# Kernel optimization log

Hardware: AMD Instinct MI355X
Metric: run time of the kernel (lower is better)

## Reference

```python
import jax, jax.numpy as jnp
import numpy as np

B, S, R, L, Z = 2048, 277, 80, 12, 56


def setup_inputs() -> dict:
    key = jax.random.key(0)
    k0, k1, k2, k3, k4, k5 = jax.random.split(key, 6)
    true_idx = jax.random.randint(k0, (B, S), 0, R)
    x = jax.nn.one_hot(true_idx, R, dtype=jnp.float32)            # one-hot true rules
    recon_x = jax.nn.softmax(jax.random.normal(k1, (B, S, R)), axis=-1)  # post-softmax probs
    mu = jax.random.normal(k2, (B, Z), dtype=jnp.float32)
    log_var = jax.random.normal(k3, (B, Z), dtype=jnp.float32)
    ind_to_lhs_ind = jax.random.randint(k4, (R,), 0, L)
    masks = (jax.random.uniform(k5, (L, R)) > 0.5).astype(jnp.float32)
    # a valid grammar always allows the true rule under its own LHS mask
    masks = masks.at[ind_to_lhs_ind, jnp.arange(R)].set(1.0)
    return {"x": x, "recon_x": recon_x, "mu": mu, "log_var": log_var,
            "masks": masks, "ind_to_lhs_ind": ind_to_lhs_ind}


def reference(x, recon_x, mu, log_var, masks, ind_to_lhs_ind):
    batch_size, seq_len, n_rules = x.shape
    z_size = mu.shape[1]
    # apply_masks: fused gather + mask + renormalize (replaces B*S python loop)
    true_rule = jnp.argmax(x, axis=-1)                 # [B,S]
    mask = masks[ind_to_lhs_ind[true_rule]]            # [B,S,R]
    x_resc = recon_x * mask
    out = x_resc / jnp.sum(x_resc, axis=-1, keepdims=True)
    # BCELoss(size_average=False): torch clamps log terms at -100
    log_p = jnp.clip(jnp.log(out), -100.0, None)
    log_1mp = jnp.clip(jnp.log1p(-out), -100.0, None)
    bce = -jnp.sum(x * log_p + (1.0 - x) * log_1mp) / (seq_len * batch_size)
    # sample_z == False branch: moment-matching error
    avg_mu = jnp.sum(mu, axis=0) / batch_size          # [Z]
    var = jnp.matmul(mu.T, mu) / batch_size            # [Z,Z]
    var_err = var - jnp.eye(z_size, dtype=mu.dtype)
    mom_err = jnp.sum(avg_mu * avg_mu) / z_size + jnp.sum(jnp.abs(var_err)) / (z_size * z_size)
    return bce + mom_err
```

## Files before the change

### kernel.cpp

```cpp
#include <hip/hip_runtime.h>
#include <math.h>

#define Bn 2048
#define Sn 277
#define Rn 80
#define Ln 12
#define Zn 56
#define NROWS (Bn * Sn)
#define NBLK_BCE 2216
#define ITERS 4
#define NMOM 32
#define MROWS (Bn / NMOM)
#define NBLK_TOT (NBLK_BCE + NMOM)
#define NWAVE_BCE (NBLK_BCE * 4)

#define WS_CM  0
#define WS_BCE 1280
#define WS_VAR 36736
#define WS_AVG 49280

typedef float f4 __attribute__((ext_vector_type(4)));

__device__ __forceinline__ float qsum4(float v) {
    int t = __builtin_amdgcn_update_dpp(0, __float_as_int(v), 0xB1, 0xF, 0xF, true);
    v += __int_as_float(t);
    t = __builtin_amdgcn_update_dpp(0, __float_as_int(v), 0x4E, 0xF, 0xF, true);
    v += __int_as_float(t);
    return v;
}

__global__ __launch_bounds__(256) void setup_kernel(
    const float* __restrict__ masks, const int* __restrict__ lhs, char* __restrict__ ws)
{
    unsigned* cmask_sw = (unsigned*)(ws + WS_CM);
    for (int idx = threadIdx.x; idx < Rn * 4; idx += 256) {
        const int r = idx >> 2, c = idx & 3;
        const int l = lhs[r];
        unsigned bits = 0u;
        for (int k = 0; k < 5; ++k)
            for (int comp = 0; comp < 4; ++comp) {
                const int j = 16 * k + 4 * c + comp;
                if (masks[l * Rn + j] > 0.5f) bits |= (1u << (4 * k + comp));
            }
        cmask_sw[idx] = bits;
    }
}

__global__ __launch_bounds__(256, 4) void main_kernel(
    const float* __restrict__ x, const float* __restrict__ recon,
    const float* __restrict__ mu, char* __restrict__ ws)
{
    const int tid = threadIdx.x;

    if (blockIdx.x < NMOM) {
        __shared__ float sm[MROWS * Zn];
        float* var_g = (float*)(ws + WS_VAR);
        float* avg_g = (float*)(ws + WS_AVG);
        const int m = blockIdx.x;
        const float* src = mu + (size_t)m * MROWS * Zn;
        for (int i = tid; i < MROWS * Zn; i += 256) sm[i] = src[i];
        __syncthreads();

        #pragma unroll 1
        for (int k = 0; k < 13; ++k) {
            const int p = tid + 256 * k;
            if (p < Zn * Zn) {
                const int i = p / Zn, j = p - i * Zn;
                float a = 0.0f;
                #pragma unroll 8
                for (int r = 0; r < MROWS; ++r) a = fmaf(sm[r * Zn + i], sm[r * Zn + j], a);
                atomicAdd(&var_g[p], a);
            }
        }
        if (tid < Zn) {
            float s = 0.0f;
            #pragma unroll 8
            for (int r = 0; r < MROWS; ++r) s += sm[r * Zn + tid];
            atomicAdd(&avg_g[tid], s);
        }
        return;
    }

    const int bid = blockIdx.x - NMOM;
    const unsigned* cmask_sw = (const unsigned*)(ws + WS_CM);
    float* bce_partial = (float*)(ws + WS_BCE);

    const int q = tid >> 2;
    const int c = tid & 3;
    const f4* xp = (const f4*)x;
    const f4* rp = (const f4*)recon;
    int off = (bid * 256 + q) * 20 + c;

    auto dotc = [](const f4 v, float base_) {
        return fmaf(v.x, base_, fmaf(v.y, base_ + 1.f, fmaf(v.z, base_ + 2.f, v.w * (base_ + 3.f))));
    };

    float ss = 0.0f;
    #pragma unroll 1
    for (int it = 0; it < ITERS; ++it, off += 64 * 20) {
        f4 X[5], Rv[5];
        #pragma unroll
        for (int k = 0; k < 5; ++k) X[k]  = __builtin_nontemporal_load(&xp[off + 4 * k]);
        #pragma unroll
        for (int k = 0; k < 5; ++k) Rv[k] = __builtin_nontemporal_load(&rp[off + 4 * k]);
        __builtin_amdgcn_sched_barrier(0);

        float dl = dotc(X[0], 0.f) + dotc(X[1], 16.f) + dotc(X[2], 32.f)
                 + dotc(X[3], 48.f) + dotc(X[4], 64.f);
        float xs = 0.f;
        #pragma unroll
        for (int k = 0; k < 5; ++k)
            xs += ((X[k].x + X[k].y) + (X[k].z + X[k].w));
        dl = fmaf((float)(4 * c), xs, dl);
        const int amax = (int)(qsum4(dl) + 0.5f);

        const unsigned bits = cmask_sw[(amax << 2) | c];

        #pragma unroll
        for (int k = 0; k < 5; ++k) {
            Rv[k].x = ((bits >> (4 * k + 0)) & 1u) ? Rv[k].x : 0.f;
            Rv[k].y = ((bits >> (4 * k + 1)) & 1u) ? Rv[k].y : 0.f;
            Rv[k].z = ((bits >> (4 * k + 2)) & 1u) ? Rv[k].z : 0.f;
            Rv[k].w = ((bits >> (4 * k + 3)) & 1u) ? Rv[k].w : 0.f;
        }
        float dd = 0.f;
        #pragma unroll
        for (int k = 0; k < 5; ++k)
            dd += ((Rv[k].x + Rv[k].y) + (Rv[k].z + Rv[k].w));
        const float invd = __builtin_amdgcn_rcpf(qsum4(dd));

        const int ka = amax >> 4;
        const int ca = (amax >> 2) & 3;
        const int comp = amax & 3;
        const bool owner = (c == ca);

        float p = 1.0f;
        float ta = 1.0f;
        #pragma unroll
        for (int k = 0; k < 5; ++k) {
            const float t0 = fminf(Rv[k].x * invd, 1.f);
            const float t1 = fminf(Rv[k].y * invd, 1.f);
            const float t2 = fminf(Rv[k].z * invd, 1.f);
            const float t3 = fminf(Rv[k].w * invd, 1.f);
            p *= ((1.f - t0) * (1.f - t1)) * ((1.f - t2) * (1.f - t3));
            if (owner && k == ka)
                ta = (comp == 0) ? t0 : (comp == 1) ? t1 : (comp == 2) ? t2 : t3;
        }
        if (p > 0.0f) {
            ss += __builtin_amdgcn_logf(p) * 0.69314718055994531f;
        } else {
            #pragma unroll
            for (int k = 0; k < 5; ++k) {
                ss += fmaxf(__logf(1.f - fminf(Rv[k].x * invd, 1.f)), -100.f)
                    + fmaxf(__logf(1.f - fminf(Rv[k].y * invd, 1.f)), -100.f)
                    + fmaxf(__logf(1.f - fminf(Rv[k].z * invd, 1.f)), -100.f)
                    + fmaxf(__logf(1.f - fminf(Rv[k].w * invd, 1.f)), -100.f);
            }
        }
        if (owner)
            ss += fmaxf(__logf(ta), -100.f) - fmaxf(__logf(1.f - ta), -100.f);
    }

    ss = qsum4(ss);
    ss += __shfl_xor(ss, 4);
    ss += __shfl_xor(ss, 8);
    ss += __shfl_xor(ss, 16);
    ss += __shfl_xor(ss, 32);
    if ((tid & 63) == 0)
        bce_partial[bid * 4 + (tid >> 6)] = ss;
}

__global__ __launch_bounds__(256) void finalize_kernel(
    const char* __restrict__ ws, float* __restrict__ out)
{
    const float* bce_partial = (const float*)(ws + WS_BCE);
    const float* var_g = (const float*)(ws + WS_VAR);
    const float* avg_g = (const float*)(ws + WS_AVG);
    __shared__ double sb[4];
    __shared__ float sv[4], sa[4];
    const int tid = threadIdx.x;

    double bsum = 0.0;
    for (int i = tid; i < NWAVE_BCE; i += 256) bsum += (double)bce_partial[i];

    float vsum = 0.0f;
    for (int p = tid; p < Zn * Zn; p += 256) {
        const int i = p / Zn, j = p - i * Zn;
        const float e = var_g[p] * (1.0f / (float)Bn) - ((i == j) ? 1.0f : 0.0f);
        vsum += fabsf(e);
    }
    float asum = 0.0f;
    for (int z = tid; z < Zn; z += 256) { const float a = avg_g[z]; asum += a * a; }

    #pragma unroll
    for (int o = 32; o; o >>= 1) {
        bsum += __shfl_xor(bsum, o);
        vsum += __shfl_xor(vsum, o);
        asum += __shfl_xor(asum, o);
    }
    if ((tid & 63) == 0) { const int w = tid >> 6; sb[w] = bsum; sv[w] = vsum; sa[w] = asum; }
    __syncthreads();
    if (tid == 0) {
        const double tb = (sb[0] + sb[1]) + (sb[2] + sb[3]);
        const double tv = (double)((sv[0] + sv[1]) + (sv[2] + sv[3]));
        const double ta = (double)((sa[0] + sa[1]) + (sa[2] + sa[3]));
        const double bce = -tb / ((double)Sn * (double)Bn);
        const double mom = ta / ((double)Bn * (double)Bn * (double)Zn)
                         + tv / ((double)Zn * (double)Zn);
        out[0] = (float)(bce + mom);
    }
}

extern "C" void kernel_launch(void* const* d_in, const int* in_sizes, int n_in,
                              void* d_out, int out_size, void* d_ws, size_t ws_size,
                              hipStream_t stream)
{
    const float* x     = (const float*)d_in[0];
    const float* recon = (const float*)d_in[1];
    const float* mu    = (const float*)d_in[2];
    const float* masks = (const float*)d_in[4];
    const int*   lhs   = (const int*)d_in[5];
    float* out = (float*)d_out;
    char* ws = (char*)d_ws;

    hipMemsetAsync(ws + WS_VAR, 0, 12544 + 224, stream);
    setup_kernel<<<1, 256, 0, stream>>>(masks, lhs, ws);
    main_kernel<<<NBLK_TOT, 256, 0, stream>>>(x, recon, mu, ws);
    finalize_kernel<<<1, 256, 0, stream>>>(ws, out);
}
```

Baseline: 361.9 us.

## Stage BCE tiles through LDS with fully coalesced loads, one tile per block

Each BCE block now handles 64 rows in a single pass instead of looping four times. It loads x and recon with fully contiguous per-thread float4 accesses, stages them in padded LDS (stride 21) to avoid bank conflicts, then reads them back in the row-per-quad layout. Partial sums are reduced per block through LDS, so there is one partial per block instead of one per wave. The aim is better global coalescing and more blocks in flight. The cost is 43KB of LDS per block, a lower occupancy hint (3), and an extra LDS round trip and barriers.

```diff
diff --git a/kernel.cpp b/kernel.cpp
--- a/kernel.cpp
+++ b/kernel.cpp
@@ -7,12 +7,11 @@
 #define Ln 12
 #define Zn 56
 #define NROWS (Bn * Sn)
-#define NBLK_BCE 2216
-#define ITERS 4
+#define ROWS_PER_BLK 64
+#define NBLK_BCE (NROWS / ROWS_PER_BLK)
 #define NMOM 32
 #define MROWS (Bn / NMOM)
 #define NBLK_TOT (NBLK_BCE + NMOM)
-#define NWAVE_BCE (NBLK_BCE * 4)
 
 #define WS_CM  0
 #define WS_BCE 1280
@@ -46,16 +45,17 @@
     }
 }
 
-__global__ __launch_bounds__(256, 4) void main_kernel(
+__global__ __launch_bounds__(256, 3) void main_kernel(
     const float* __restrict__ x, const float* __restrict__ recon,
     const float* __restrict__ mu, char* __restrict__ ws)
 {
+    __shared__ f4 ldsb[2688];
     const int tid = threadIdx.x;
 
     if (blockIdx.x < NMOM) {
-        __shared__ float sm[MROWS * Zn];
         float* var_g = (float*)(ws + WS_VAR);
         float* avg_g = (float*)(ws + WS_AVG);
+        float* sm = (float*)ldsb;
         const int m = blockIdx.x;
         const float* src = mu + (size_t)m * MROWS * Zn;
         for (int i = tid; i < MROWS * Zn; i += 256) sm[i] = src[i];
@@ -85,26 +85,40 @@
     const unsigned* cmask_sw = (const unsigned*)(ws + WS_CM);
     float* bce_partial = (float*)(ws + WS_BCE);
 
-    const int q = tid >> 2;
-    const int c = tid & 3;
-    const f4* xp = (const f4*)x;
-    const f4* rp = (const f4*)recon;
-    int off = (bid * 256 + q) * 20 + c;
+    const size_t base = (size_t)bid * (ROWS_PER_BLK * (Rn / 4));
+    const f4* xg = (const f4*)x + base;
+    const f4* rg = (const f4*)recon + base;
+
+    f4 tv[10];
+    #pragma unroll
+    for (int i = 0; i < 5; ++i) tv[i]     = __builtin_nontemporal_load(&xg[256 * i + tid]);
+    #pragma unroll
+    for (int i = 0; i < 5; ++i) tv[5 + i] = __builtin_nontemporal_load(&rg[256 * i + tid]);
+    #pragma unroll
+    for (int i = 0; i < 5; ++i) {
+        const int f = 256 * i + tid;
+        const int row = f / 20, col = f - 20 * row;
+        ldsb[row * 21 + col]        = tv[i];
+        ldsb[1344 + row * 21 + col] = tv[5 + i];
+    }
+    __syncthreads();
+
+    const int qq = tid >> 2;
+    const int c  = tid & 3;
+    const int sb = qq * 21 + c;
+
+    f4 X[5], Rv[5];
+    #pragma unroll
+    for (int k = 0; k < 5; ++k) X[k]  = ldsb[sb + 4 * k];
+    #pragma unroll
+    for (int k = 0; k < 5; ++k) Rv[k] = ldsb[1344 + sb + 4 * k];
 
     auto dotc = [](const f4 v, float base_) {
         return fmaf(v.x, base_, fmaf(v.y, base_ + 1.f, fmaf(v.z, base_ + 2.f, v.w * (base_ + 3.f))));
     };
 
     float ss = 0.0f;
-    #pragma unroll 1
-    for (int it = 0; it < ITERS; ++it, off += 64 * 20) {
-        f4 X[5], Rv[5];
-        #pragma unroll
-        for (int k = 0; k < 5; ++k) X[k]  = __builtin_nontemporal_load(&xp[off + 4 * k]);
-        #pragma unroll
-        for (int k = 0; k < 5; ++k) Rv[k] = __builtin_nontemporal_load(&rp[off + 4 * k]);
-        __builtin_amdgcn_sched_barrier(0);
-
+    {
         float dl = dotc(X[0], 0.f) + dotc(X[1], 16.f) + dotc(X[2], 32.f)
                  + dotc(X[3], 48.f) + dotc(X[4], 64.f);
         float xs = 0.f;
@@ -166,8 +180,12 @@
     ss += __shfl_xor(ss, 8);
     ss += __shfl_xor(ss, 16);
     ss += __shfl_xor(ss, 32);
-    if ((tid & 63) == 0)
-        bce_partial[bid * 4 + (tid >> 6)] = ss;
+    __syncthreads();
+    float* smf = (float*)ldsb;
+    if ((tid & 63) == 0) smf[tid >> 6] = ss;
+    __syncthreads();
+    if (tid == 0)
+        bce_partial[bid] = (smf[0] + smf[1]) + (smf[2] + smf[3]);
 }
 
 __global__ __launch_bounds__(256) void finalize_kernel(
@@ -181,7 +199,7 @@
     const int tid = threadIdx.x;
 
     double bsum = 0.0;
-    for (int i = tid; i < NWAVE_BCE; i += 256) bsum += (double)bce_partial[i];
+    for (int i = tid; i < NBLK_BCE; i += 256) bsum += (double)bce_partial[i];
 
     float vsum = 0.0f;
     for (int p = tid; p < Zn * Zn; p += 256) {
```

Result: faster. 354.3 us, median of 2 (-2.1%).
